# Performance work log

Measured on AMD Instinct MI355X. Metric: run time of the kernel, lower is better.

The kernel has to match this reference:

```python
import jax, jax.numpy as jnp
import numpy as np

EMB = 256
B, C, H, W = 8, EMB, 64, 64
TOPK = 150


def setup_inputs() -> dict:
    key = jax.random.key(0)
    k1, k2, k3, k4 = jax.random.split(key, 4)
    img_feat = jax.random.normal(k1, (B, C, H, W), dtype=jnp.float32)
    exe_feat = jax.random.normal(k2, (B, C), dtype=jnp.float32)
    # similarity is initialized to identity in the module; add small noise so the
    # bilinear form is non-trivial for kernel correctness testing
    similarity = jnp.eye(EMB, dtype=jnp.float32) + 0.02 * jax.random.normal(k3, (EMB, EMB), dtype=jnp.float32)
    # torch nn.Linear(C, C, bias=False): y = x @ W.T, W shape (out, in)
    v_weight = jax.random.normal(k4, (EMB, EMB), dtype=jnp.float32) * (1.0 / np.sqrt(EMB))
    return {"img_feat": img_feat, "exe_feat": exe_feat, "similarity": similarity, "v_weight": v_weight}


def reference(img_feat, exe_feat, similarity, v_weight):
    Bs, Cs, Hs, Ws = img_feat.shape
    HWp = Hs * Ws
    unrolled = img_feat.reshape(Bs, Cs, HWp)                      # B,C,HW
    exe = (exe_feat * 1.2)[:, :, None]                            # B,C,1
    concat = jnp.concatenate([unrolled, exe], axis=2)             # B,C,HW+1
    # values = Linear(v) applied to concat^T: (B,HW+1,C) @ W^T
    values = jnp.einsum('bcn,dc->bnd', concat, v_weight)          # B,HW+1,C
    # bilinear attention scores: unrolled^T @ S @ concat
    proj = jnp.einsum('bcm,cd->bmd', unrolled, similarity)        # B,HW,C
    attn = jnp.einsum('bmd,bdn->bmn', proj, concat)               # B,HW,HW+1
    sim_w_exe = attn[:, :, -1]                                    # B,HW (score vs exemplar)
    _, q_ids = jax.lax.top_k(sim_w_exe, TOPK)                     # B,150
    vals_pos = values[:, :-1, :]                                  # B,HW,C (drop exemplar slot)
    queries = jnp.take_along_axis(vals_pos, q_ids[:, :, None], axis=1)  # B,150,C
    attn_sm = jax.nn.softmax(attn, axis=2)                        # B,HW,HW+1
    new_img_feat = jnp.einsum('bmn,bnd->bmd', attn_sm, values)    # B,HW,C
    return new_img_feat, queries
```

## Files before the change

kernel.cpp:

```cpp
#include <hip/hip_runtime.h>

typedef _Float16 f16;
typedef _Float16 f16x8 __attribute__((ext_vector_type(8)));
typedef float f32x4 __attribute__((ext_vector_type(4)));

#define NB 8
#define NC 256
#define NHW 4096
#define NPADN 4160
#define NTOPK 150

__global__ __launch_bounds__(256) void k_prep1(const float* __restrict__ exe,
                                               const float* __restrict__ sim,
                                               double* __restrict__ tvec,
                                               f16* __restrict__ Kt) {
  int b = blockIdx.x, c = threadIdx.x;
  __shared__ double e[NC];
  double v = (double)exe[b*NC + c] * 1.2;
  e[c] = v;
  Kt[((size_t)b*NPADN + NHW)*NC + c] = (f16)(float)v;
  for (int r = NHW + 1; r < NPADN; ++r)
    Kt[((size_t)b*NPADN + r)*NC + c] = (f16)0.f;
  __syncthreads();
  double acc = 0.0;
  for (int d = 0; d < NC; ++d) acc += (double)sim[c*NC + d] * e[d];
  tvec[b*NC + c] = acc;
}

__global__ __launch_bounds__(256) void k_small(const float* __restrict__ sim,
                                               const float* __restrict__ vw,
                                               f16* __restrict__ simT,
                                               f16* __restrict__ Wh) {
  int cc = blockIdx.x, d = threadIdx.x;
  simT[d*NC + cc] = (f16)sim[cc*NC + d];
  Wh[cc*NC + d]   = (f16)vw[cc*NC + d];
}

__global__ __launch_bounds__(256) void k_transpose(const float* __restrict__ img,
                                                   const double* __restrict__ tvec,
                                                   f16* __restrict__ Kt,
                                                   double* __restrict__ swe4) {
  __shared__ float tile[64][65];
  __shared__ double red[64][5];
  int n0 = blockIdx.x*64, c0 = blockIdx.y*64, b = blockIdx.z;
  int t = threadIdx.x;
#pragma unroll
  for (int i = 0; i < 16; ++i) {
    int cl = (t>>6) + 4*i, nl = t&63;
    tile[cl][nl] = img[((size_t)b*NC + c0+cl)*NHW + n0 + nl];
  }
  __syncthreads();
#pragma unroll
  for (int i = 0; i < 16; ++i) {
    int nl = (t>>6) + 4*i, cl = t&63;
    Kt[((size_t)b*NPADN + n0+nl)*NC + c0 + cl] = (f16)tile[cl][nl];
  }
  {
    int m = t&63, q = t>>6;
    double p = 0.0;
#pragma unroll
    for (int i = 0; i < 16; ++i) {
      int cl = q*16 + i;
      p += (double)tile[cl][m] * tvec[b*NC + c0 + cl];
    }
    red[m][q] = p;
  }
  __syncthreads();
  if (t < 64) {
    double s = red[t][0] + red[t][1] + red[t][2] + red[t][3];
    swe4[((size_t)(b*4 + blockIdx.y))*NHW + n0 + t] = s;
  }
}

__global__ __launch_bounds__(256) void k_qgemm(const f16* __restrict__ Kt,
                                               const f16* __restrict__ simT,
                                               f16* __restrict__ Q) {
  int b = blockIdx.y, m0 = blockIdx.x*64;
  int tid = threadIdx.x, w = tid>>6, l = tid&63, lm = l&15, g = l>>4;
  __shared__ f16 KtL[64*256];
  {
    const char* src = (const char*)(Kt + ((size_t)b*NPADN + m0)*NC);
#pragma unroll
    for (int p = 0; p < 8; ++p) {
      int row = p*8 + (tid>>5), c16 = tid&31;
      *(f16x8*)((char*)KtL + row*512 + ((c16*16) ^ ((row&7)<<4))) =
          *(const f16x8*)(src + row*512 + c16*16);
    }
  }
  __syncthreads();
  f16x8 a[8];
#pragma unroll
  for (int k = 0; k < 8; ++k) {
    int row = w*16 + lm;
    a[k] = *(const f16x8*)((const char*)KtL + row*512 + ((k*64 + g*16) ^ ((row&7)<<4)));
  }
  f32x4 acc[16];
#pragma unroll
  for (int i = 0; i < 16; ++i) acc[i] = (f32x4){0.f,0.f,0.f,0.f};
#pragma unroll
  for (int dt = 0; dt < 16; ++dt) {
    const f16* bb = simT + (size_t)(dt*16 + lm)*NC + g*8;
#pragma unroll
    for (int k = 0; k < 8; ++k) {
      f16x8 bf = *(const f16x8*)(bb + k*32);
      acc[dt] = __builtin_amdgcn_mfma_f32_16x16x32_f16(a[k], bf, acc[dt], 0,0,0);
    }
  }
  __syncthreads();
  f16* outl = KtL;
#pragma unroll
  for (int dt = 0; dt < 16; ++dt)
#pragma unroll
    for (int r = 0; r < 4; ++r)
      outl[(w*16 + g*4 + r)*256 + dt*16 + lm] = (f16)acc[dt][r];
  __syncthreads();
  f16* dst = Q + ((size_t)b*NHW + m0)*NC;
#pragma unroll
  for (int p = 0; p < 8; ++p) {
    int row = p*8 + (tid>>5), c16 = tid&31;
    *(f16x8*)((char*)dst + row*512 + c16*16) =
        *(const f16x8*)((const char*)outl + row*512 + c16*16);
  }
}

__global__ __launch_bounds__(256) void k_vgemm(const f16* __restrict__ Kt,
                                               const f16* __restrict__ Wh,
                                               const int* __restrict__ qids,
                                               f16* __restrict__ Vt,
                                               float* __restrict__ outQ) {
  int b = blockIdx.y, n0 = blockIdx.x*64;
  int tid = threadIdx.x, w = tid>>6, l = tid&63, lm = l&15, g = l>>4;
  __shared__ f16 KtL[4*64*72];
  __shared__ int qid_s[NTOPK];
  if (tid < NTOPK) qid_s[tid] = qids[b*NTOPK + tid];
  {
    const char* src = (const char*)(Kt + ((size_t)b*NPADN + n0)*NC);
#pragma unroll
    for (int p = 0; p < 8; ++p) {
      int row = p*8 + (tid>>5), c16 = tid&31;
      *(f16x8*)((char*)KtL + row*512 + ((c16*16) ^ ((row&7)<<4))) =
          *(const f16x8*)(src + row*512 + c16*16);
    }
  }
  __syncthreads();
  f32x4 acc[4][4];
#pragma unroll
  for (int i = 0; i < 4; ++i)
#pragma unroll
    for (int j = 0; j < 4; ++j) acc[i][j] = (f32x4){0.f,0.f,0.f,0.f};
#pragma unroll
  for (int k = 0; k < 8; ++k) {
    f16x8 bf[4];
#pragma unroll
    for (int nt = 0; nt < 4; ++nt) {
      int row = nt*16 + lm;
      bf[nt] = *(const f16x8*)((const char*)KtL + row*512 + ((k*64 + g*16) ^ ((row&7)<<4)));
    }
#pragma unroll
    for (int dt = 0; dt < 4; ++dt) {
      f16x8 af = *(const f16x8*)(Wh + (size_t)(w*64 + dt*16 + lm)*NC + k*32 + g*8);
#pragma unroll
      for (int nt = 0; nt < 4; ++nt)
        acc[dt][nt] = __builtin_amdgcn_mfma_f32_16x16x32_f16(af, bf[nt], acc[dt][nt], 0,0,0);
    }
  }
  __syncthreads();
  f16* outl = KtL + w*4608;
#pragma unroll
  for (int dt = 0; dt < 4; ++dt)
#pragma unroll
    for (int nt = 0; nt < 4; ++nt)
#pragma unroll
      for (int r = 0; r < 4; ++r)
        outl[(dt*16 + g*4 + r)*72 + nt*16 + lm] = (f16)acc[dt][nt][r];
  __syncthreads();
  {
    f16* dst = Vt + ((size_t)(b*NC + w*64 + l))*NPADN + n0;
    const f16* srcl = outl + l*72;
#pragma unroll
    for (int c16 = 0; c16 < 8; ++c16)
      *(f16x8*)((char*)dst + c16*16) = *(const f16x8*)((const char*)srcl + c16*16);
  }
  for (int j = 0; j < NTOPK; ++j) {
    int nl = qid_s[j] - n0;
    if (nl >= 0 && nl < 64) {
      int w2 = tid>>6, dl = tid&63;
      outQ[((size_t)b*NTOPK + j)*NC + tid] = (float)KtL[w2*4608 + dl*72 + nl];
    }
  }
}

__global__ __launch_bounds__(256) void k_topk(const double* __restrict__ swe4,
                                              double* __restrict__ swe,
                                              int* __restrict__ qids) {
  int b = blockIdx.x, tid = threadIdx.x, w = tid>>6, l = tid&63;
  __shared__ double vals[NHW];
  __shared__ double rv[4];
  __shared__ int ri[4];
#pragma unroll
  for (int j = 0; j < 16; ++j) {
    int idx = j*256 + tid;
    double s = swe4[((size_t)(b*4 + 0))*NHW + idx] + swe4[((size_t)(b*4 + 1))*NHW + idx]
             + swe4[((size_t)(b*4 + 2))*NHW + idx] + swe4[((size_t)(b*4 + 3))*NHW + idx];
    vals[idx] = s;
    swe[(size_t)b*NHW + idx] = s;
  }
  __syncthreads();
  for (int k = 0; k < NTOPK; ++k) {
    double bv = -1e300; int bi = 0x7fffffff;
    for (int j = 0; j < 16; ++j) {
      int idx = j*256 + tid;
      double v = vals[idx];
      if (v > bv || (v == bv && idx < bi)) { bv = v; bi = idx; }
    }
#pragma unroll
    for (int off = 1; off < 64; off <<= 1) {
      double ov = __shfl_xor(bv, off);
      int oi = __shfl_xor(bi, off);
      if (ov > bv || (ov == bv && oi < bi)) { bv = ov; bi = oi; }
    }
    if (l == 0) { rv[w] = bv; ri[w] = bi; }
    __syncthreads();
    double fv = rv[0]; int fi = ri[0];
#pragma unroll
    for (int x = 1; x < 4; ++x)
      if (rv[x] > fv || (rv[x] == fv && ri[x] < fi)) { fv = rv[x]; fi = ri[x]; }
    if (tid == 0) qids[b*NTOPK + k] = fi;
    if ((fi & 255) == tid) vals[fi] = -1e300;
    __syncthreads();
  }
}

__global__ __launch_bounds__(256) void k_flash(const f16* __restrict__ Q,
                                               const f16* __restrict__ Kt,
                                               const f16* __restrict__ Vt,
                                               const double* __restrict__ swe,
                                               float* __restrict__ outI) {
  int bid = blockIdx.x;
  int b = bid & 7;
  int m0 = (bid >> 3) * 64;
  int tid = threadIdx.x, w = tid>>6, l = tid&63, lm = l&15, g = l>>4;

  __shared__ f16 KL[64*256];
  __shared__ f16 VL[256*64];
  __shared__ f16 PL[64*72];
  __shared__ f16 vex[256];

  vex[tid] = Vt[((size_t)(b*NC + tid))*NPADN + NHW];

  f16x8 q[8];
  {
    const f16* qp = Q + ((size_t)b*NHW + m0 + w*16 + lm)*NC + g*8;
#pragma unroll
    for (int k = 0; k < 8; ++k) q[k] = *(const f16x8*)(qp + k*32);
  }
  f32x4 acc[16];
#pragma unroll
  for (int i = 0; i < 16; ++i) acc[i] = (f32x4){0.f,0.f,0.f,0.f};
  float mrun[4], lrun[4];
#pragma unroll
  for (int r = 0; r < 4; ++r) { mrun[r] = -1e30f; lrun[r] = 0.f; }

  const int krow = tid>>5, kc16 = tid&31;
  const int vrow = tid>>3, vc16 = tid&7;
  const char* Ksrc = (const char*)(Kt + ((size_t)b*NPADN)*NC);
  const char* Vsrc = (const char*)(Vt + ((size_t)b*NC)*NPADN);
  f16x8 gk[8], gv[8];

#pragma unroll
  for (int p = 0; p < 8; ++p)
    gk[p] = *(const f16x8*)(Ksrc + (size_t)(p*8 + krow)*512 + kc16*16);
#pragma unroll
  for (int p = 0; p < 8; ++p)
    gv[p] = *(const f16x8*)(Vsrc + (size_t)(p*32 + vrow)*(NPADN*2) + vc16*16);
#pragma unroll
  for (int p = 0; p < 8; ++p) {
    int row = p*8 + krow;
    *(f16x8*)((char*)KL + row*512 + ((kc16*16) ^ ((row&7)<<4))) = gk[p];
  }
#pragma unroll
  for (int p = 0; p < 8; ++p) {
    int row = p*32 + vrow;
    *(f16x8*)((char*)VL + row*128 + ((vc16*16) ^ ((row&7)<<4))) = gv[p];
  }

  for (int t = 0; t < 64; ++t) {
    __syncthreads();
    if (t < 63) {
      size_t n1 = (size_t)(t+1)*64;
#pragma unroll
      for (int p = 0; p < 8; ++p)
        gk[p] = *(const f16x8*)(Ksrc + (n1 + p*8 + krow)*512 + kc16*16);
#pragma unroll
      for (int p = 0; p < 8; ++p)
        gv[p] = *(const f16x8*)(Vsrc + (size_t)(p*32 + vrow)*(NPADN*2) + n1*2 + vc16*16);
    }
    f32x4 s[4];
#pragma unroll
    for (int nt = 0; nt < 4; ++nt) s[nt] = (f32x4){0.f,0.f,0.f,0.f};
#pragma unroll
    for (int k = 0; k < 8; ++k) {
#pragma unroll
      for (int nt = 0; nt < 4; ++nt) {
        int row = nt*16 + lm;
        f16x8 bf = *(const f16x8*)((const char*)KL + row*512 + ((k*64 + g*16) ^ ((row&7)<<4)));
        s[nt] = __builtin_amdgcn_mfma_f32_16x16x32_f16(q[k], bf, s[nt], 0,0,0);
      }
    }
    float mx[4];
#pragma unroll
    for (int r = 0; r < 4; ++r) {
      float m2 = fmaxf(fmaxf(s[0][r], s[1][r]), fmaxf(s[2][r], s[3][r]));
#pragma unroll
      for (int off = 1; off < 16; off <<= 1) m2 = fmaxf(m2, __shfl_xor(m2, off));
      mx[r] = m2;
    }
    bool grow = (mx[0] > mrun[0]) | (mx[1] > mrun[1]) | (mx[2] > mrun[2]) | (mx[3] > mrun[3]);
    if (__ballot(grow)) {
#pragma unroll
      for (int r = 0; r < 4; ++r) {
        float mnew = fmaxf(mrun[r], mx[r]);
        float scale = __expf(mrun[r] - mnew);
        mrun[r] = mnew;
        lrun[r] *= scale;
#pragma unroll
        for (int dt = 0; dt < 16; ++dt) acc[dt][r] *= scale;
      }
    }
#pragma unroll
    for (int r = 0; r < 4; ++r) {
      float rs = 0.f;
#pragma unroll
      for (int nt = 0; nt < 4; ++nt) {
        float p = __expf(s[nt][r] - mrun[r]);
        s[nt][r] = p;
        rs += p;
      }
#pragma unroll
      for (int off = 1; off < 16; off <<= 1) rs += __shfl_xor(rs, off);
      lrun[r] += rs;
    }
#pragma unroll
    for (int nt = 0; nt < 4; ++nt)
#pragma unroll
      for (int r = 0; r < 4; ++r)
        PL[(w*16 + g*4 + r)*72 + nt*16 + lm] = (f16)s[nt][r];
#pragma unroll
    for (int ks = 0; ks < 2; ++ks) {
      f16x8 pa = *(const f16x8*)((const char*)PL + (w*16 + lm)*144 + ks*64 + g*16);
#pragma unroll
      for (int dt = 0; dt < 16; ++dt) {
        int row = dt*16 + lm;
        f16x8 vf = *(const f16x8*)((const char*)VL + row*128 + ((ks*64 + g*16) ^ ((row&7)<<4)));
        acc[dt] = __builtin_amdgcn_mfma_f32_16x16x32_f16(pa, vf, acc[dt], 0,0,0);
      }
    }
    __syncthreads();
    if (t < 63) {
#pragma unroll
      for (int p = 0; p < 8; ++p) {
        int row = p*8 + krow;
        *(f16x8*)((char*)KL + row*512 + ((kc16*16) ^ ((row&7)<<4))) = gk[p];
      }
#pragma unroll
      for (int p = 0; p < 8; ++p) {
        int row = p*32 + vrow;
        *(f16x8*)((char*)VL + row*128 + ((vc16*16) ^ ((row&7)<<4))) = gv[p];
      }
    }
  }
#pragma unroll
  for (int r = 0; r < 4; ++r) {
    float sv = (float)swe[(size_t)b*NHW + m0 + w*16 + g*4 + r];
    float mnew = fmaxf(mrun[r], sv);
    float scale = __expf(mrun[r] - mnew);
    float pe = __expf(sv - mnew);
    mrun[r] = mnew;
    lrun[r] = lrun[r]*scale + pe;
#pragma unroll
    for (int dt = 0; dt < 16; ++dt)
      acc[dt][r] = acc[dt][r]*scale + pe * (float)vex[dt*16 + lm];
  }
  float* dst = outI + ((size_t)b*NHW + m0 + w*16)*NC;
#pragma unroll
  for (int dt = 0; dt < 16; ++dt)
#pragma unroll
    for (int r = 0; r < 4; ++r)
      dst[(size_t)(g*4 + r)*NC + dt*16 + lm] = acc[dt][r] / lrun[r];
}

extern "C" void kernel_launch(void* const* d_in, const int* in_sizes, int n_in,
                              void* d_out, int out_size, void* d_ws, size_t ws_size,
                              hipStream_t stream) {
  const float* img = (const float*)d_in[0];
  const float* exe = (const float*)d_in[1];
  const float* sim = (const float*)d_in[2];
  const float* vw  = (const float*)d_in[3];
  float* out = (float*)d_out;
  char* ws = (char*)d_ws;

  f16*    Kt   = (f16*)(ws);
  f16*    Q    = (f16*)(ws + 17039360);
  f16*    Vt   = (f16*)(ws + 33816576);
  f16*    simT = (f16*)(ws + 50855936);
  f16*    Wh   = (f16*)(ws + 50987008);
  double* tvec = (double*)(ws + 51118080);
  double* swe  = (double*)(ws + 51134464);
  int*    qids = (int*)(ws + 51396608);
  double* swe4 = (double*)(ws + 51401472);

  float* outImg = out;
  float* outQ   = out + (size_t)NB*NHW*NC;

  k_prep1<<<dim3(NB), dim3(256), 0, stream>>>(exe, sim, tvec, Kt);
  k_small<<<dim3(256), dim3(256), 0, stream>>>(sim, vw, simT, Wh);
  k_transpose<<<dim3(64,4,NB), dim3(256), 0, stream>>>(img, tvec, Kt, swe4);
  k_topk<<<dim3(NB), dim3(256), 0, stream>>>(swe4, swe, qids);
  k_qgemm<<<dim3(64,NB), dim3(256), 0, stream>>>(Kt, simT, Q);
  k_vgemm<<<dim3(65,NB), dim3(256), 0, stream>>>(Kt, Wh, qids, Vt, outQ);
  k_flash<<<dim3(512), dim3(256), 0, stream>>>(Q, Kt, Vt, swe, outImg);
}
```

Baseline: 833.1 us.

## Read K/V fragments directly from global memory and keep top-k candidates in registers

The flash-attention kernel no longer stages K and V tiles through LDS with register prefetch and double barriers. Each wave now loads its MFMA B-operand fragments straight from global memory, relying on L1/L2 caching to share data across the four waves. This cuts LDS traffic, one barrier per tile and register pressure, but exposes global-load latency with no explicit prefetch and issues redundant loads from every wave. Separately, top-k keeps each thread's 16 candidates in registers with a cached per-thread max, uses double-buffered reduction slots to drop a barrier, and rescans only in the thread that owned the selected element.

```diff
diff --git a/kernel.cpp b/kernel.cpp
--- a/kernel.cpp
+++ b/kernel.cpp
@@ -194,40 +194,46 @@
                                               double* __restrict__ swe,
                                               int* __restrict__ qids) {
   int b = blockIdx.x, tid = threadIdx.x, w = tid>>6, l = tid&63;
-  __shared__ double vals[NHW];
-  __shared__ double rv[4];
-  __shared__ int ri[4];
+  __shared__ double rv[2][4];
+  __shared__ int    ri[2][4];
+  double v[16];
 #pragma unroll
   for (int j = 0; j < 16; ++j) {
     int idx = j*256 + tid;
     double s = swe4[((size_t)(b*4 + 0))*NHW + idx] + swe4[((size_t)(b*4 + 1))*NHW + idx]
              + swe4[((size_t)(b*4 + 2))*NHW + idx] + swe4[((size_t)(b*4 + 3))*NHW + idx];
-    vals[idx] = s;
+    v[j] = s;
     swe[(size_t)b*NHW + idx] = s;
   }
-  __syncthreads();
+  double bv = v[0]; int bj = 0;
+#pragma unroll
+  for (int j = 1; j < 16; ++j) if (v[j] > bv) { bv = v[j]; bj = j; }
+  int bi = bj*256 + tid;
+
   for (int k = 0; k < NTOPK; ++k) {
-    double bv = -1e300; int bi = 0x7fffffff;
-    for (int j = 0; j < 16; ++j) {
-      int idx = j*256 + tid;
-      double v = vals[idx];
-      if (v > bv || (v == bv && idx < bi)) { bv = v; bi = idx; }
-    }
+    int p = k & 1;
+    double mv = bv; int mi = bi;
 #pragma unroll
     for (int off = 1; off < 64; off <<= 1) {
-      double ov = __shfl_xor(bv, off);
-      int oi = __shfl_xor(bi, off);
-      if (ov > bv || (ov == bv && oi < bi)) { bv = ov; bi = oi; }
-    }
-    if (l == 0) { rv[w] = bv; ri[w] = bi; }
+      double ov = __shfl_xor(mv, off);
+      int oi = __shfl_xor(mi, off);
+      if (ov > mv || (ov == mv && oi < mi)) { mv = ov; mi = oi; }
+    }
+    if (l == 0) { rv[p][w] = mv; ri[p][w] = mi; }
     __syncthreads();
-    double fv = rv[0]; int fi = ri[0];
+    double fv = rv[p][0]; int fi = ri[p][0];
 #pragma unroll
     for (int x = 1; x < 4; ++x)
-      if (rv[x] > fv || (rv[x] == fv && ri[x] < fi)) { fv = rv[x]; fi = ri[x]; }
+      if (rv[p][x] > fv || (rv[p][x] == fv && ri[p][x] < fi)) { fv = rv[p][x]; fi = ri[p][x]; }
     if (tid == 0) qids[b*NTOPK + k] = fi;
-    if ((fi & 255) == tid) vals[fi] = -1e300;
-    __syncthreads();
+    if ((fi & 255) == tid) {
+#pragma unroll
+      for (int j = 0; j < 16; ++j) if (fi == j*256 + tid) v[j] = -1e300;
+      bv = v[0]; bj = 0;
+#pragma unroll
+      for (int j = 1; j < 16; ++j) if (v[j] > bv) { bv = v[j]; bj = j; }
+      bi = bj*256 + tid;
+    }
   }
 }
 
@@ -241,12 +247,10 @@
   int m0 = (bid >> 3) * 64;
   int tid = threadIdx.x, w = tid>>6, l = tid&63, lm = l&15, g = l>>4;
 
-  __shared__ f16 KL[64*256];
-  __shared__ f16 VL[256*64];
   __shared__ f16 PL[64*72];
-  __shared__ f16 vex[256];
-
-  vex[tid] = Vt[((size_t)(b*NC + tid))*NPADN + NHW];
+
+  const f16* Kb = Kt + (size_t)b*NPADN*NC;
+  const f16* Vb = Vt + (size_t)b*NC*NPADN;
 
   f16x8 q[8];
   {
@@ -261,40 +265,8 @@
 #pragma unroll
   for (int r = 0; r < 4; ++r) { mrun[r] = -1e30f; lrun[r] = 0.f; }
 
-  const int krow = tid>>5, kc16 = tid&31;
-  const int vrow = tid>>3, vc16 = tid&7;
-  const char* Ksrc = (const char*)(Kt + ((size_t)b*NPADN)*NC);
-  const char* Vsrc = (const char*)(Vt + ((size_t)b*NC)*NPADN);
-  f16x8 gk[8], gv[8];
-
-#pragma unroll
-  for (int p = 0; p < 8; ++p)
-    gk[p] = *(const f16x8*)(Ksrc + (size_t)(p*8 + krow)*512 + kc16*16);
-#pragma unroll
-  for (int p = 0; p < 8; ++p)
-    gv[p] = *(const f16x8*)(Vsrc + (size_t)(p*32 + vrow)*(NPADN*2) + vc16*16);
-#pragma unroll
-  for (int p = 0; p < 8; ++p) {
-    int row = p*8 + krow;
-    *(f16x8*)((char*)KL + row*512 + ((kc16*16) ^ ((row&7)<<4))) = gk[p];
-  }
-#pragma unroll
-  for (int p = 0; p < 8; ++p) {
-    int row = p*32 + vrow;
-    *(f16x8*)((char*)VL + row*128 + ((vc16*16) ^ ((row&7)<<4))) = gv[p];
-  }
-
-  for (int t = 0; t < 64; ++t) {
-    __syncthreads();
-    if (t < 63) {
-      size_t n1 = (size_t)(t+1)*64;
-#pragma unroll
-      for (int p = 0; p < 8; ++p)
-        gk[p] = *(const f16x8*)(Ksrc + (n1 + p*8 + krow)*512 + kc16*16);
-#pragma unroll
-      for (int p = 0; p < 8; ++p)
-        gv[p] = *(const f16x8*)(Vsrc + (size_t)(p*32 + vrow)*(NPADN*2) + n1*2 + vc16*16);
-    }
+  for (int n0 = 0; n0 < NHW; n0 += 64) {
+    __builtin_amdgcn_s_barrier();
     f32x4 s[4];
 #pragma unroll
     for (int nt = 0; nt < 4; ++nt) s[nt] = (f32x4){0.f,0.f,0.f,0.f};
@@ -302,8 +274,7 @@
     for (int k = 0; k < 8; ++k) {
 #pragma unroll
       for (int nt = 0; nt < 4; ++nt) {
-        int row = nt*16 + lm;
-        f16x8 bf = *(const f16x8*)((const char*)KL + row*512 + ((k*64 + g*16) ^ ((row&7)<<4)));
+        f16x8 bf = *(const f16x8*)(Kb + (size_t)(n0 + nt*16 + lm)*NC + k*32 + g*8);
         s[nt] = __builtin_amdgcn_mfma_f32_16x16x32_f16(q[k], bf, s[nt], 0,0,0);
       }
     }
@@ -350,22 +321,8 @@
       f16x8 pa = *(const f16x8*)((const char*)PL + (w*16 + lm)*144 + ks*64 + g*16);
 #pragma unroll
       for (int dt = 0; dt < 16; ++dt) {
-        int row = dt*16 + lm;
-        f16x8 vf = *(const f16x8*)((const char*)VL + row*128 + ((ks*64 + g*16) ^ ((row&7)<<4)));
+        f16x8 vf = *(const f16x8*)(Vb + (size_t)(dt*16 + lm)*NPADN + n0 + ks*32 + g*8);
         acc[dt] = __builtin_amdgcn_mfma_f32_16x16x32_f16(pa, vf, acc[dt], 0,0,0);
-      }
-    }
-    __syncthreads();
-    if (t < 63) {
-#pragma unroll
-      for (int p = 0; p < 8; ++p) {
-        int row = p*8 + krow;
-        *(f16x8*)((char*)KL + row*512 + ((kc16*16) ^ ((row&7)<<4))) = gk[p];
-      }
-#pragma unroll
-      for (int p = 0; p < 8; ++p) {
-        int row = p*32 + vrow;
-        *(f16x8*)((char*)VL + row*128 + ((vc16*16) ^ ((row&7)<<4))) = gv[p];
       }
     }
   }
@@ -378,8 +335,10 @@
     mrun[r] = mnew;
     lrun[r] = lrun[r]*scale + pe;
 #pragma unroll
-    for (int dt = 0; dt < 16; ++dt)
-      acc[dt][r] = acc[dt][r]*scale + pe * (float)vex[dt*16 + lm];
+    for (int dt = 0; dt < 16; ++dt) {
+      float vex = (float)Vb[(size_t)(dt*16 + lm)*NPADN + NHW];
+      acc[dt][r] = acc[dt][r]*scale + pe * vex;
+    }
   }
   float* dst = outI + ((size_t)b*NHW + m0 + w*16)*NC;
 #pragma unroll
```

After: 1.354 ms. 62.5% more time.
